# Performance work log

Measured on AMD Instinct MI355X. Metric: run time of the kernel, lower is better.

## Reference

```python
import jax, jax.numpy as jnp
import numpy as np

B, C, NF, L = 4, 16, 10000, 100000


def setup_inputs() -> dict:
    key = jax.random.key(0)
    k0, k1, k2, k3, k4, k5 = jax.random.split(key, 6)
    i_f = jax.random.normal(k0, (B, C, NF, 2), dtype=jnp.float32)
    i_s = jax.random.normal(k1, (B, C, L, 2), dtype=jnp.float32)
    t_f = jax.random.normal(k2, (B, C, NF, 2), dtype=jnp.float32)
    t_s = jax.random.normal(k3, (B, C, L, 2), dtype=jnp.float32)
    xi_idx = jax.random.randint(k4, (L, 2), 0, NF, dtype=jnp.int64)
    ks = jax.random.normal(k5, (L, 2), dtype=jnp.float32)
    return {"i_f": i_f, "i_s": i_s, "t_f": t_f, "t_s": t_s,
            "xi_idx": xi_idx, "ks": ks}


def _cmul_conj(a, b):
    # a * conj(b) with last dim = (real, imag); matches cplx.mul(a, cplx.conjugate(b))
    ar, ai = a[..., 0], a[..., 1]
    br, bi = b[..., 0], b[..., 1]
    return jnp.stack([ar * br + ai * bi, ai * br - ar * bi], axis=-1)


def reference(i_f, i_s, t_f, t_s, xi_idx, ks):
    f_gap = i_f - t_f            # [B,C,NF,2]
    s_gap = i_s - t_s            # [B,C,L,2]
    idx0, idx1 = xi_idx[:, 0], xi_idx[:, 1]
    # masked_fill(idx_null, 0): zero where ks > 0; broadcast [1,1,L,1]
    m0 = (ks[:, 0] > 0)[None, None, :, None]
    m1 = (ks[:, 1] > 0)[None, None, :, None]
    zero = jnp.zeros((), dtype=f_gap.dtype)
    f0 = jnp.where(m0, zero, f_gap[:, :, idx0])   # [B,C,L,2]
    f1 = jnp.where(m1, zero, f_gap[:, :, idx1])
    tf0 = jnp.where(m0, zero, t_f[:, :, idx0])
    tf1 = jnp.where(m1, zero, t_f[:, :, idx1])
    g = s_gap - _cmul_conj(f0, tf1) - _cmul_conj(tf0, f1)  # [B,C,L,2]
    # mse_norm: sum of squares over complex dim, mean over everything else
    return jnp.mean(jnp.sum(g * g, axis=-1))
```

## Files before the change

### kernel.cpp

```cpp
#include <hip/hip_runtime.h>

#define NB 4
#define NC 16
#define NF 10000
#define LL 100000

typedef float f32x2 __attribute__((ext_vector_type(2)));

constexpr int BC = NB * NC;
constexpr int BLOCK = 256;
constexpr int TL = 64;
constexpr int NBLK = (LL + TL - 1) / TL;
constexpr int CSTR = 65;

constexpr size_t WS_ACC   = 0;
constexpr size_t WS_FGAPT = 256;
constexpr size_t WS_TFT   = 256 + (size_t)NF * 64 * 8;
constexpr size_t WS_NEED  = WS_TFT + (size_t)NF * 64 * 8;

__global__ __launch_bounds__(256) void transpose_prep(
    const float2* __restrict__ i_f, const float2* __restrict__ t_f,
    float2* __restrict__ fgap_t, float2* __restrict__ tft)
{
    __shared__ float2 tg[64][65];
    __shared__ float2 tt[64][65];
    const int nf0  = blockIdx.x * 64;
    const int nrem = min(64, NF - nf0);
    const int lane = threadIdx.x & 63;
    const int q    = threadIdx.x >> 6;
    if (lane < nrem) {
        for (int bc = q; bc < BC; bc += 4) {
            float2 iv = i_f[(size_t)bc * NF + nf0 + lane];
            float2 tv = t_f[(size_t)bc * NF + nf0 + lane];
            tg[bc][lane] = make_float2(iv.x - tv.x, iv.y - tv.y);
            tt[bc][lane] = tv;
        }
    }
    __syncthreads();
    for (int j = q; j < nrem; j += 4) {
        fgap_t[(size_t)(nf0 + j) * BC + lane] = tg[lane][j];
        tft  [(size_t)(nf0 + j) * BC + lane] = tt[lane][j];
    }
}

__global__ __launch_bounds__(BLOCK) void mse_main2(
    const float* __restrict__ i_s, const float* __restrict__ t_s,
    const int2*  __restrict__ xi,  const float2* __restrict__ ks,
    const float2* __restrict__ fgap_t, const float2* __restrict__ tft,
    double* __restrict__ acc)
{
    __shared__ float2 corr[TL * CSTR];
    __shared__ int2   xi_list[TL];
    __shared__ int    pos[TL];
    __shared__ int    cnt;
    __shared__ float  wsum[BLOCK / 64];

    const int l0   = blockIdx.x * TL;
    const int tlb  = min(TL, LL - l0);
    const int lane = threadIdx.x & 63;
    const int wid  = threadIdx.x >> 6;
    const int tid  = threadIdx.x;

    if (tid == 0) cnt = 0;
    if (tid < TL) pos[tid] = -1;
    __syncthreads();

    if (tid < tlb) {
        float2 k = ks[l0 + tid];
        if (!(k.x > 0.f) && !(k.y > 0.f)) {
            int slot = atomicAdd(&cnt, 1);
            pos[tid] = slot;
            xi_list[slot] = xi[l0 + tid];
        }
    }
    __syncthreads();

    const int nact = cnt;
    for (int a = wid; a < nact; a += BLOCK / 64) {
        int2 idx = xi_list[a];
        float2 f0  = fgap_t[(size_t)idx.x * BC + lane];
        float2 tf1 = tft  [(size_t)idx.y * BC + lane];
        float2 tf0 = tft  [(size_t)idx.x * BC + lane];
        float2 f1  = fgap_t[(size_t)idx.y * BC + lane];
        float cr = f0.x * tf1.x + f0.y * tf1.y + tf0.x * f1.x + tf0.y * f1.y;
        float ci = f0.y * tf1.x - f0.x * tf1.y + tf0.y * f1.x - tf0.x * f1.y;
        corr[a * CSTR + lane] = make_float2(cr, ci);
    }
    __syncthreads();

    float sum = 0.f;
    if (lane < tlb) {
        const int l = l0 + lane;
        const int myslot = pos[lane];
        for (int bc = wid; bc < BC; bc += BLOCK / 64) {
            const f32x2* ip = (const f32x2*)(i_s + 2 * ((size_t)bc * LL + l));
            const f32x2* tp = (const f32x2*)(t_s + 2 * ((size_t)bc * LL + l));
            f32x2 si = __builtin_nontemporal_load(ip);
            f32x2 st = __builtin_nontemporal_load(tp);
            float gr = si.x - st.x;
            float gi = si.y - st.y;
            if (myslot >= 0) {
                float2 cc = corr[myslot * CSTR + bc];
                gr -= cc.x;
                gi -= cc.y;
            }
            sum += gr * gr + gi * gi;
        }
    }

    #pragma unroll
    for (int off = 32; off; off >>= 1) sum += __shfl_down(sum, off, 64);
    if (lane == 0) wsum[wid] = sum;
    __syncthreads();
    if (tid == 0) {
        float t = wsum[0] + wsum[1] + wsum[2] + wsum[3];
        atomicAdd(acc, (double)t);
    }
}

constexpr int FCHUNKS = 32;
constexpr int FCHUNK  = (LL + FCHUNKS - 1) / FCHUNKS;

__global__ __launch_bounds__(BLOCK) void mse_fallback(
    const float* __restrict__ i_f, const float* __restrict__ i_s,
    const float* __restrict__ t_f, const float* __restrict__ t_s,
    const int*  __restrict__ xi,  const float* __restrict__ ks,
    double* __restrict__ acc)
{
    const int bc    = blockIdx.x / FCHUNKS;
    const int chunk = blockIdx.x % FCHUNKS;
    const int l0 = chunk * FCHUNK;
    const int l1 = (l0 + FCHUNK < LL) ? (l0 + FCHUNK) : LL;

    const float2* isv = (const float2*)i_s + (size_t)bc * LL;
    const float2* tsv = (const float2*)t_s + (size_t)bc * LL;
    const float2* ifv = (const float2*)i_f + (size_t)bc * NF;
    const float2* tfv = (const float2*)t_f + (size_t)bc * NF;
    const int2*   xiv = (const int2*)xi;
    const float2* ksv = (const float2*)ks;

    float sum = 0.f;
    for (int l = l0 + (int)threadIdx.x; l < l1; l += BLOCK) {
        float2 si = isv[l], st = tsv[l];
        float gr = si.x - st.x, gi = si.y - st.y;
        float2 k = ksv[l];
        if (!(k.x > 0.f) && !(k.y > 0.f)) {
            int2 idx = xiv[l];
            float2 tf0 = tfv[idx.x], if0 = ifv[idx.x];
            float2 tf1 = tfv[idx.y], if1 = ifv[idx.y];
            float f0r = if0.x - tf0.x, f0i = if0.y - tf0.y;
            float f1r = if1.x - tf1.x, f1i = if1.y - tf1.y;
            gr -= f0r * tf1.x + f0i * tf1.y;
            gi -= f0i * tf1.x - f0r * tf1.y;
            gr -= tf0.x * f1r + tf0.y * f1i;
            gi -= tf0.y * f1r - tf0.x * f1i;
        }
        sum += gr * gr + gi * gi;
    }
    #pragma unroll
    for (int off = 32; off; off >>= 1) sum += __shfl_down(sum, off, 64);
    __shared__ float ws[BLOCK / 64];
    const int lane = threadIdx.x & 63, wwid = threadIdx.x >> 6;
    if (lane == 0) ws[wwid] = sum;
    __syncthreads();
    if (threadIdx.x == 0) {
        float t = 0.f;
        #pragma unroll
        for (int i = 0; i < BLOCK / 64; ++i) t += ws[i];
        atomicAdd(acc, (double)t);
    }
}

__global__ void mse_finalize(const double* __restrict__ acc, float* __restrict__ out)
{
    out[0] = (float)(acc[0] / (double)((size_t)BC * LL));
}

extern "C" void kernel_launch(void* const* d_in, const int* in_sizes, int n_in,
                              void* d_out, int out_size, void* d_ws, size_t ws_size,
                              hipStream_t stream)
{
    const float* i_f = (const float*)d_in[0];
    const float* i_s = (const float*)d_in[1];
    const float* t_f = (const float*)d_in[2];
    const float* t_s = (const float*)d_in[3];
    const int*   xi  = (const int*)d_in[4];
    const float* ks  = (const float*)d_in[5];
    float* out = (float*)d_out;

    char* ws = (char*)d_ws;
    double* acc = (double*)(ws + WS_ACC);
    (void)hipMemsetAsync(acc, 0, sizeof(double), stream);

    if (ws_size >= WS_NEED) {
        float2* fgap_t = (float2*)(ws + WS_FGAPT);
        float2* tft    = (float2*)(ws + WS_TFT);
        transpose_prep<<<(NF + 63) / 64, 256, 0, stream>>>(
            (const float2*)i_f, (const float2*)t_f, fgap_t, tft);
        mse_main2<<<NBLK, BLOCK, 0, stream>>>(
            i_s, t_s, (const int2*)xi, (const float2*)ks, fgap_t, tft, acc);
    } else {
        mse_fallback<<<BC * FCHUNKS, BLOCK, 0, stream>>>(
            i_f, i_s, t_f, t_s, xi, ks, acc);
    }
    mse_finalize<<<1, 1, 0, stream>>>(acc, out);
}
```

Baseline: 62.58 us.

## Interleave gap and target tables, widen blocks, fuse finalize via last-block counter

The prep kernel now writes a single interleaved table of (f_gap, t_f) as float4 per (nf, bc), so each active column needs two 16-byte gathers instead of four 8-byte gathers. The main kernel uses 512-thread blocks with a fully unrolled channel loop, stores the correction matrix transposed in shared memory, and has the last finishing block compute the final mean through an atomic done counter, which removes the separate finalize launch. The cost is a larger prep tile footprint and a threadfence plus extra atomic per block.

```diff
diff --git a/kernel.cpp b/kernel.cpp
--- a/kernel.cpp
+++ b/kernel.cpp
@@ -1,65 +1,66 @@
 #include <hip/hip_runtime.h>
 
-#define NB 4
-#define NC 16
 #define NF 10000
 #define LL 100000
 
 typedef float f32x2 __attribute__((ext_vector_type(2)));
-
-constexpr int BC = NB * NC;
-constexpr int BLOCK = 256;
-constexpr int TL = 64;
-constexpr int NBLK = (LL + TL - 1) / TL;
-constexpr int CSTR = 65;
-
-constexpr size_t WS_ACC   = 0;
-constexpr size_t WS_FGAPT = 256;
-constexpr size_t WS_TFT   = 256 + (size_t)NF * 64 * 8;
-constexpr size_t WS_NEED  = WS_TFT + (size_t)NF * 64 * 8;
-
-__global__ __launch_bounds__(256) void transpose_prep(
+typedef float f32x4 __attribute__((ext_vector_type(4)));
+
+constexpr int BC    = 64;
+constexpr int TL    = 64;
+constexpr int NBLK  = (LL + TL - 1) / TL;
+constexpr int BLOCK = 512;
+constexpr int NW    = BLOCK / 64;
+constexpr int CSTR  = 65;
+
+constexpr int TNF   = 32;
+constexpr int TBLK  = (NF + TNF - 1) / TNF;
+
+constexpr size_t WS_ACC  = 0;
+constexpr size_t WS_DONE = 8;
+constexpr size_t WS_TBL  = 256;
+constexpr size_t WS_NEED = WS_TBL + (size_t)NF * BC * 16;
+
+__global__ __launch_bounds__(256) void prep_t(
     const float2* __restrict__ i_f, const float2* __restrict__ t_f,
-    float2* __restrict__ fgap_t, float2* __restrict__ tft)
-{
-    __shared__ float2 tg[64][65];
-    __shared__ float2 tt[64][65];
-    const int nf0  = blockIdx.x * 64;
-    const int nrem = min(64, NF - nf0);
+    f32x4* __restrict__ tbl)
+{
+    __shared__ f32x4 t4[BC][TNF + 1];
+    const int nf0  = blockIdx.x * TNF;
+    const int nrem = min(TNF, NF - nf0);
+    const int c = threadIdx.x & 31;
+    const int r = threadIdx.x >> 5;
+    if (c < nrem) {
+        for (int bc = r; bc < BC; bc += 8) {
+            float2 iv = i_f[(size_t)bc * NF + nf0 + c];
+            float2 tv = t_f[(size_t)bc * NF + nf0 + c];
+            t4[bc][c] = (f32x4){iv.x - tv.x, iv.y - tv.y, tv.x, tv.y};
+        }
+    }
+    __syncthreads();
     const int lane = threadIdx.x & 63;
-    const int q    = threadIdx.x >> 6;
-    if (lane < nrem) {
-        for (int bc = q; bc < BC; bc += 4) {
-            float2 iv = i_f[(size_t)bc * NF + nf0 + lane];
-            float2 tv = t_f[(size_t)bc * NF + nf0 + lane];
-            tg[bc][lane] = make_float2(iv.x - tv.x, iv.y - tv.y);
-            tt[bc][lane] = tv;
-        }
-    }
-    __syncthreads();
-    for (int j = q; j < nrem; j += 4) {
-        fgap_t[(size_t)(nf0 + j) * BC + lane] = tg[lane][j];
-        tft  [(size_t)(nf0 + j) * BC + lane] = tt[lane][j];
-    }
-}
-
-__global__ __launch_bounds__(BLOCK) void mse_main2(
+    const int w    = threadIdx.x >> 6;
+    for (int j = w; j < nrem; j += 4)
+        tbl[(size_t)(nf0 + j) * BC + lane] = t4[lane][j];
+}
+
+__global__ __launch_bounds__(BLOCK) void mse_main3(
     const float* __restrict__ i_s, const float* __restrict__ t_s,
     const int2*  __restrict__ xi,  const float2* __restrict__ ks,
-    const float2* __restrict__ fgap_t, const float2* __restrict__ tft,
-    double* __restrict__ acc)
-{
-    __shared__ float2 corr[TL * CSTR];
+    const f32x4* __restrict__ tbl,
+    double* __restrict__ acc, int* __restrict__ done, float* __restrict__ out)
+{
+    __shared__ float2 corr[BC * CSTR];
     __shared__ int2   xi_list[TL];
     __shared__ int    pos[TL];
     __shared__ int    cnt;
-    __shared__ float  wsum[BLOCK / 64];
+    __shared__ float  wsum[NW];
 
     const int l0   = blockIdx.x * TL;
     const int tlb  = min(TL, LL - l0);
-    const int lane = threadIdx.x & 63;
-    const int wid  = threadIdx.x >> 6;
     const int tid  = threadIdx.x;
+    const int lane = tid & 63;
+    const int wid  = tid >> 6;
 
     if (tid == 0) cnt = 0;
     if (tid < TL) pos[tid] = -1;
@@ -76,15 +77,13 @@
     __syncthreads();
 
     const int nact = cnt;
-    for (int a = wid; a < nact; a += BLOCK / 64) {
+    for (int a = wid; a < nact; a += NW) {
         int2 idx = xi_list[a];
-        float2 f0  = fgap_t[(size_t)idx.x * BC + lane];
-        float2 tf1 = tft  [(size_t)idx.y * BC + lane];
-        float2 tf0 = tft  [(size_t)idx.x * BC + lane];
-        float2 f1  = fgap_t[(size_t)idx.y * BC + lane];
-        float cr = f0.x * tf1.x + f0.y * tf1.y + tf0.x * f1.x + tf0.y * f1.y;
-        float ci = f0.y * tf1.x - f0.x * tf1.y + tf0.y * f1.x - tf0.x * f1.y;
-        corr[a * CSTR + lane] = make_float2(cr, ci);
+        f32x4 r0 = tbl[(size_t)idx.x * BC + lane];
+        f32x4 r1 = tbl[(size_t)idx.y * BC + lane];
+        float cr = r0.x * r1.z + r0.y * r1.w + r0.z * r1.x + r0.w * r1.y;
+        float ci = r0.y * r1.z - r0.x * r1.w + r0.w * r1.x - r0.z * r1.y;
+        corr[lane * CSTR + a] = make_float2(cr, ci);
     }
     __syncthreads();
 
@@ -92,15 +91,15 @@
     if (lane < tlb) {
         const int l = l0 + lane;
         const int myslot = pos[lane];
-        for (int bc = wid; bc < BC; bc += BLOCK / 64) {
-            const f32x2* ip = (const f32x2*)(i_s + 2 * ((size_t)bc * LL + l));
-            const f32x2* tp = (const f32x2*)(t_s + 2 * ((size_t)bc * LL + l));
-            f32x2 si = __builtin_nontemporal_load(ip);
-            f32x2 st = __builtin_nontemporal_load(tp);
+        #pragma unroll
+        for (int it = 0; it < BC / NW; ++it) {
+            const int bc = wid + it * NW;
+            f32x2 si = __builtin_nontemporal_load((const f32x2*)(i_s + 2 * ((size_t)bc * LL + l)));
+            f32x2 st = __builtin_nontemporal_load((const f32x2*)(t_s + 2 * ((size_t)bc * LL + l)));
             float gr = si.x - st.x;
             float gi = si.y - st.y;
             if (myslot >= 0) {
-                float2 cc = corr[myslot * CSTR + bc];
+                float2 cc = corr[bc * CSTR + myslot];
                 gr -= cc.x;
                 gi -= cc.y;
             }
@@ -113,15 +112,23 @@
     if (lane == 0) wsum[wid] = sum;
     __syncthreads();
     if (tid == 0) {
-        float t = wsum[0] + wsum[1] + wsum[2] + wsum[3];
+        float t = 0.f;
+        #pragma unroll
+        for (int i = 0; i < NW; ++i) t += wsum[i];
         atomicAdd(acc, (double)t);
+        __threadfence();
+        int prev = atomicAdd(done, 1);
+        if (prev == NBLK - 1) {
+            double total = atomicAdd(acc, 0.0);
+            out[0] = (float)(total / (double)((size_t)BC * LL));
+        }
     }
 }
 
 constexpr int FCHUNKS = 32;
 constexpr int FCHUNK  = (LL + FCHUNKS - 1) / FCHUNKS;
 
-__global__ __launch_bounds__(BLOCK) void mse_fallback(
+__global__ __launch_bounds__(256) void mse_fallback(
     const float* __restrict__ i_f, const float* __restrict__ i_s,
     const float* __restrict__ t_f, const float* __restrict__ t_s,
     const int*  __restrict__ xi,  const float* __restrict__ ks,
@@ -140,7 +147,7 @@
     const float2* ksv = (const float2*)ks;
 
     float sum = 0.f;
-    for (int l = l0 + (int)threadIdx.x; l < l1; l += BLOCK) {
+    for (int l = l0 + (int)threadIdx.x; l < l1; l += 256) {
         float2 si = isv[l], st = tsv[l];
         float gr = si.x - st.x, gi = si.y - st.y;
         float2 k = ksv[l];
@@ -159,14 +166,12 @@
     }
     #pragma unroll
     for (int off = 32; off; off >>= 1) sum += __shfl_down(sum, off, 64);
-    __shared__ float ws[BLOCK / 64];
+    __shared__ float ws[4];
     const int lane = threadIdx.x & 63, wwid = threadIdx.x >> 6;
     if (lane == 0) ws[wwid] = sum;
     __syncthreads();
     if (threadIdx.x == 0) {
-        float t = 0.f;
-        #pragma unroll
-        for (int i = 0; i < BLOCK / 64; ++i) t += ws[i];
+        float t = ws[0] + ws[1] + ws[2] + ws[3];
         atomicAdd(acc, (double)t);
     }
 }
@@ -190,18 +195,17 @@
 
     char* ws = (char*)d_ws;
     double* acc = (double*)(ws + WS_ACC);
-    (void)hipMemsetAsync(acc, 0, sizeof(double), stream);
+    int*   done = (int*)(ws + WS_DONE);
+    (void)hipMemsetAsync(ws, 0, 16, stream);
 
     if (ws_size >= WS_NEED) {
-        float2* fgap_t = (float2*)(ws + WS_FGAPT);
-        float2* tft    = (float2*)(ws + WS_TFT);
-        transpose_prep<<<(NF + 63) / 64, 256, 0, stream>>>(
-            (const float2*)i_f, (const float2*)t_f, fgap_t, tft);
-        mse_main2<<<NBLK, BLOCK, 0, stream>>>(
-            i_s, t_s, (const int2*)xi, (const float2*)ks, fgap_t, tft, acc);
+        f32x4* tbl = (f32x4*)(ws + WS_TBL);
+        prep_t<<<TBLK, 256, 0, stream>>>((const float2*)i_f, (const float2*)t_f, tbl);
+        mse_main3<<<NBLK, BLOCK, 0, stream>>>(
+            i_s, t_s, (const int2*)xi, (const float2*)ks, tbl, acc, done, out);
     } else {
-        mse_fallback<<<BC * FCHUNKS, BLOCK, 0, stream>>>(
+        mse_fallback<<<BC * FCHUNKS, 256, 0, stream>>>(
             i_f, i_s, t_f, t_s, xi, ks, acc);
-    }
-    mse_finalize<<<1, 1, 0, stream>>>(acc, out);
-}
+        mse_finalize<<<1, 1, 0, stream>>>(acc, out);
+    }
+}
```

Result: slower. 96.13 us (+53.6%).
